# Kernel tuning notes

Hardware: AMD Instinct MI355X
Metric: run time of the kernel (lower is better)

## Reference

```python
import jax, jax.numpy as jnp
import numpy as np

B, L, D = 2, 2048, 1024
H = 16
DH = D // H
DFF = 4096
THETA = 10000.0
EPS = 1e-5


def setup_inputs() -> dict:
    key = jax.random.key(0)
    ks = jax.random.split(key, 6)
    s_qkv = (2.0 / (D + 3 * D)) ** 0.5
    s_o = (2.0 / (D + D)) ** 0.5
    s_ff = (2.0 / (D + DFF)) ** 0.5
    return {
        'x': jax.random.normal(ks[0], (B, L, D), jnp.float32),
        'w_qkv': jax.random.normal(ks[1], (3 * D, D), jnp.float32) * s_qkv,
        'w_o': jax.random.normal(ks[2], (D, D), jnp.float32) * s_o,
        'w1': jax.random.normal(ks[3], (DFF, D), jnp.float32) * s_ff,
        'w2': jax.random.normal(ks[4], (D, DFF), jnp.float32) * s_ff,
        'w3': jax.random.normal(ks[5], (DFF, D), jnp.float32) * s_ff,
        'g1': jnp.ones((D,), jnp.float32),
        'g2': jnp.ones((D,), jnp.float32),
    }


def _rmsnorm(x, g):
    xf = x.astype(jnp.float32)
    inv = jax.lax.rsqrt(jnp.mean(xf * xf, axis=-1, keepdims=True) + EPS)
    return (xf * inv * g).astype(x.dtype)


def _rotate_pair(t):
    # interleaved pairs: (x0,x1,x2,x3,...) -> (-x1,x0,-x3,x2,...)
    t2 = t.reshape(t.shape[:-1] + (t.shape[-1] // 2, 2))
    r = jnp.stack((-t2[..., 1], t2[..., 0]), axis=-1)
    return r.reshape(t.shape)


def reference(x, w_qkv, w_o, w1, w2, w3, g1, g2):
    Bb, Ll, Dd = x.shape
    # --- attention sublayer ---
    y = _rmsnorm(x, g1)
    qkv = y @ w_qkv.T                       # (B, L, 3D)
    q, k, v = jnp.split(qkv, 3, axis=-1)
    def to_heads(t):
        return t.reshape(Bb, Ll, H, DH).transpose(0, 2, 1, 3)  # (B,H,L,Dh)
    q, k, v = to_heads(q), to_heads(k), to_heads(v)
    # RoPE (interleaved), positions = 0..L-1
    inv_freq = 1.0 / (THETA ** (jnp.arange(0, DH, 2, dtype=jnp.float32) / DH))
    ang = jnp.arange(Ll, dtype=jnp.float32)[:, None] * inv_freq  # (L, Dh/2)
    ang = jnp.repeat(ang, 2, axis=-1)                            # (L, Dh)
    cos, sin = jnp.cos(ang), jnp.sin(ang)
    q = q * cos + _rotate_pair(q) * sin
    k = k * cos + _rotate_pair(k) * sin
    att = jnp.einsum('bhqd,bhkd->bhqk', q, k) * (1.0 / np.sqrt(DH))
    causal = jnp.tril(jnp.ones((Ll, Ll), dtype=bool))
    att = jnp.where(causal, att, -jnp.inf)
    att = jax.nn.softmax(att, axis=-1)
    yh = jnp.einsum('bhqk,bhkd->bhqd', att, v)
    y = yh.transpose(0, 2, 1, 3).reshape(Bb, Ll, Dd)
    x = x + y @ w_o.T
    # --- SwiGLU FFN sublayer ---
    y = _rmsnorm(x, g2)
    h = jax.nn.silu(y @ w1.T) * (y @ w3.T)
    return x + h @ w2.T
```

## Files before the change

kernel.cpp:

```cpp
#include <hip/hip_runtime.h>


typedef __attribute__((ext_vector_type(8))) short short8;
typedef __attribute__((ext_vector_type(4))) float f32x4;

#define DEV __device__ __forceinline__

DEV unsigned short f2b(float f) {
  unsigned int u = __builtin_bit_cast(unsigned int, f);
  unsigned int r = u + 0x7fffu + ((u >> 16) & 1u);
  return (unsigned short)(r >> 16);
}
DEV float b2f(unsigned short h) {
  return __builtin_bit_cast(float, ((unsigned int)h) << 16);
}
DEV f32x4 MFMA(short8 a, short8 b, f32x4 c) {
  return __builtin_amdgcn_mfma_f32_16x16x32_bf16(a, b, c, 0, 0, 0);
}
DEV void gload16(const void* g, void* lds) {
  __builtin_amdgcn_global_load_lds((const __attribute__((address_space(1))) void*)g,
                                   (__attribute__((address_space(3))) void*)lds, 16, 0, 0);
}

__global__ __launch_bounds__(256) void cvt_k(const float* __restrict__ src,
                                             unsigned short* __restrict__ dst, int n) {
  int i = (blockIdx.x * 256 + threadIdx.x) * 4;
  if (i + 3 < n) {
    float4 v = *(const float4*)(src + i);
    ushort4 o;
    o.x = f2b(v.x); o.y = f2b(v.y); o.z = f2b(v.z); o.w = f2b(v.w);
    *(ushort4*)(dst + i) = o;
  } else {
    for (int c = 0; c < 4 && i + c < n; ++c) dst[i + c] = f2b(src[i + c]);
  }
}

__global__ __launch_bounds__(256) void rope_k(float2* __restrict__ tab) {
  const int i = blockIdx.x * 256 + threadIdx.x;
  const int lt = i >> 5, pr = i & 31;
  const float invf = __expf((float)pr * -0.28782313662425572f);
  const float ang = (float)lt * invf;
  float sn, cs;
  sincosf(ang, &sn, &cs);
  tab[i] = make_float2(cs, sn);
}

__global__ __launch_bounds__(256) void rms_k(const float* __restrict__ x,
                                             const float* __restrict__ g,
                                             unsigned short* __restrict__ out) {
  const int row = blockIdx.x;
  const int t = threadIdx.x;
  const float4 v = *(const float4*)(x + (size_t)row * 1024 + t * 4);
  float ss = v.x * v.x + v.y * v.y + v.z * v.z + v.w * v.w;
#pragma unroll
  for (int m = 32; m >= 1; m >>= 1) ss += __shfl_xor(ss, m, 64);
  __shared__ float red[4];
  if ((t & 63) == 0) red[t >> 6] = ss;
  __syncthreads();
  float tot = red[0] + red[1] + red[2] + red[3];
  float inv = rsqrtf(tot * (1.0f / 1024.0f) + 1e-5f);
  ushort4 o;
  o.x = f2b(v.x * inv * g[t * 4 + 0]);
  o.y = f2b(v.y * inv * g[t * 4 + 1]);
  o.z = f2b(v.z * inv * g[t * 4 + 2]);
  o.w = f2b(v.w * inv * g[t * 4 + 3]);
  *(ushort4*)(out + (size_t)row * 1024 + t * 4) = o;
}

template <int MODE>
__global__ __launch_bounds__(256, 3) void gemm_bt(
    const unsigned short* __restrict__ A, const unsigned short* __restrict__ B0,
    int M, int N, int K,
    float* __restrict__ outF, const float* __restrict__ resid,
    unsigned short* __restrict__ q, unsigned short* __restrict__ k2,
    unsigned short* __restrict__ v,
    const float2* __restrict__ rtab) {
  __shared__ __align__(16) unsigned short As[2][128 * 32];
  __shared__ __align__(16) unsigned short Bs[2][128 * 32];
  const int t = threadIdx.x;
  const int wv = t >> 6, ln = t & 63;
  const int l15 = ln & 15, grp = ln >> 4;
  const int wr = wv >> 1, wc = wv & 1;
  int m0, n0;
  if constexpr (MODE == 1) {
    const int d = blockIdx.y * 8 + blockIdx.x;
    const int xcd = d & 7, j = d >> 3;
    m0 = (xcd * 4 + (j >> 3)) * 128;
    n0 = (j & 7) * 128;
  } else {
    m0 = blockIdx.y * 128;
    n0 = blockIdx.x * 128;
  }

  const char* sA0 = (const char*)A + ((size_t)(m0 + (t >> 2)) * K + (t & 3) * 8) * 2;
  const char* sA1 = (const char*)A + ((size_t)(m0 + 64 + (t >> 2)) * K + (t & 3) * 8) * 2;
  const char* sB0 = (const char*)B0 + ((size_t)(n0 + (t >> 2)) * K + (t & 3) * 8) * 2;
  const char* sB1 = (const char*)B0 + ((size_t)(n0 + 64 + (t >> 2)) * K + (t & 3) * 8) * 2;

  f32x4 acc[4][4];
#pragma unroll
  for (int mm = 0; mm < 4; ++mm)
#pragma unroll
    for (int nn = 0; nn < 4; ++nn) acc[mm][nn] = (f32x4){0.f, 0.f, 0.f, 0.f};

  const int KT = K >> 5;
  gload16(sA0, (char*)As[0] + wv * 1024);
  gload16(sA1, (char*)As[0] + 4096 + wv * 1024);
  gload16(sB0, (char*)Bs[0] + wv * 1024);
  gload16(sB1, (char*)Bs[0] + 4096 + wv * 1024);

#pragma unroll 1
  for (int kt = 0; kt < KT; ++kt) {
    const int par = kt & 1;
    const size_t ko = (size_t)((kt + 1 < KT) ? (kt + 1) : kt) * 64;
    gload16(sA0 + ko, (char*)As[par ^ 1] + wv * 1024);
    gload16(sA1 + ko, (char*)As[par ^ 1] + 4096 + wv * 1024);
    gload16(sB0 + ko, (char*)Bs[par ^ 1] + wv * 1024);
    gload16(sB1 + ko, (char*)Bs[par ^ 1] + 4096 + wv * 1024);
    asm volatile("s_waitcnt vmcnt(4)" ::: "memory");
    __builtin_amdgcn_s_barrier();
    const unsigned short* Ab = As[par];
    const unsigned short* Bb = Bs[par];
    short8 af[4], bf0[4];
#pragma unroll
    for (int mm = 0; mm < 4; ++mm)
      af[mm] = *(const short8*)&Ab[(wr * 64 + mm * 16 + l15) * 32 + grp * 8];
#pragma unroll
    for (int nn = 0; nn < 4; ++nn)
      bf0[nn] = *(const short8*)&Bb[(wc * 64 + nn * 16 + l15) * 32 + grp * 8];
#pragma unroll
    for (int mm = 0; mm < 4; ++mm)
#pragma unroll
      for (int nn = 0; nn < 4; ++nn) acc[mm][nn] = MFMA(af[mm], bf0[nn], acc[mm][nn]);
    __builtin_amdgcn_s_barrier();
  }

#pragma unroll
  for (int mm = 0; mm < 4; ++mm)
#pragma unroll
    for (int nn = 0; nn < 4; ++nn)
#pragma unroll
      for (int j = 0; j < 4; ++j) {
        const int r = m0 + wr * 64 + mm * 16 + grp * 4 + j;
        const int c = n0 + wc * 64 + nn * 16 + l15;
        float val = acc[mm][nn][j];
        if constexpr (MODE == 0) {
          const int mat = c >> 10;
          const int rem = c & 1023;
          const int hh = rem >> 6;
          const int dh = rem & 63;
          const int bt = r >> 11;
          const int lt = r & 2047;
          float outv = val;
          if (mat < 2) {
            const float partner = __shfl_xor(val, 1, 64);
            const float2 cs = rtab[lt * 32 + (dh >> 1)];
            outv = (dh & 1) ? (val * cs.x + partner * cs.y) : (val * cs.x - partner * cs.y);
          }
          unsigned short* dst = (mat == 0) ? q : ((mat == 1) ? k2 : v);
          dst[((size_t)(bt * 16 + hh) * 2048 + lt) * 64 + dh] = f2b(outv);
        } else {
          const size_t idx = (size_t)r * N + c;
          outF[idx] = resid[idx] + val;
        }
      }
}

__global__ __launch_bounds__(256, 3) void gemm_sk(
    const unsigned short* __restrict__ A, const unsigned short* __restrict__ B0,
    unsigned short* __restrict__ part) {
  __shared__ __align__(16) unsigned short As[2][128 * 32];
  __shared__ __align__(16) unsigned short Bs[2][128 * 32];
  const int t = threadIdx.x;
  const int wv = t >> 6, ln = t & 63;
  const int l15 = ln & 15, grp = ln >> 4;
  const int wr = wv >> 1, wc = wv & 1;
  const int d = blockIdx.y * 8 + blockIdx.x;
  const int xcd = d & 7, j = d >> 3;
  const int m0 = (xcd * 4 + (j >> 3)) * 128;
  const int n0 = (j & 7) * 128;
  const size_t kbase = (size_t)blockIdx.z * 1024;

  const char* sA0 = (const char*)A + ((size_t)(m0 + (t >> 2)) * 4096 + kbase + (t & 3) * 8) * 2;
  const char* sA1 = (const char*)A + ((size_t)(m0 + 64 + (t >> 2)) * 4096 + kbase + (t & 3) * 8) * 2;
  const char* sB0 = (const char*)B0 + ((size_t)(n0 + (t >> 2)) * 4096 + kbase + (t & 3) * 8) * 2;
  const char* sB1 = (const char*)B0 + ((size_t)(n0 + 64 + (t >> 2)) * 4096 + kbase + (t & 3) * 8) * 2;

  f32x4 acc[4][4];
#pragma unroll
  for (int mm = 0; mm < 4; ++mm)
#pragma unroll
    for (int nn = 0; nn < 4; ++nn) acc[mm][nn] = (f32x4){0.f, 0.f, 0.f, 0.f};

  gload16(sA0, (char*)As[0] + wv * 1024);
  gload16(sA1, (char*)As[0] + 4096 + wv * 1024);
  gload16(sB0, (char*)Bs[0] + wv * 1024);
  gload16(sB1, (char*)Bs[0] + 4096 + wv * 1024);

#pragma unroll 1
  for (int kt = 0; kt < 32; ++kt) {
    const int par = kt & 1;
    const size_t ko = (size_t)((kt + 1 < 32) ? (kt + 1) : kt) * 64;
    gload16(sA0 + ko, (char*)As[par ^ 1] + wv * 1024);
    gload16(sA1 + ko, (char*)As[par ^ 1] + 4096 + wv * 1024);
    gload16(sB0 + ko, (char*)Bs[par ^ 1] + wv * 1024);
    gload16(sB1 + ko, (char*)Bs[par ^ 1] + 4096 + wv * 1024);
    asm volatile("s_waitcnt vmcnt(4)" ::: "memory");
    __builtin_amdgcn_s_barrier();
    const unsigned short* Ab = As[par];
    const unsigned short* Bb = Bs[par];
    short8 af[4], bf0[4];
#pragma unroll
    for (int mm = 0; mm < 4; ++mm)
      af[mm] = *(const short8*)&Ab[(wr * 64 + mm * 16 + l15) * 32 + grp * 8];
#pragma unroll
    for (int nn = 0; nn < 4; ++nn)
      bf0[nn] = *(const short8*)&Bb[(wc * 64 + nn * 16 + l15) * 32 + grp * 8];
#pragma unroll
    for (int mm = 0; mm < 4; ++mm)
#pragma unroll
      for (int nn = 0; nn < 4; ++nn) acc[mm][nn] = MFMA(af[mm], bf0[nn], acc[mm][nn]);
    __builtin_amdgcn_s_barrier();
  }

  unsigned short* pz = part + (size_t)blockIdx.z * 4194304;
#pragma unroll
  for (int mm = 0; mm < 4; ++mm)
#pragma unroll
    for (int nn = 0; nn < 4; ++nn)
#pragma unroll
      for (int j = 0; j < 4; ++j) {
        const int r = m0 + wr * 64 + mm * 16 + grp * 4 + j;
        const int c = n0 + wc * 64 + nn * 16 + l15;
        pz[(size_t)r * 1024 + c] = f2b(acc[mm][nn][j]);
      }
}

__global__ __launch_bounds__(256) void red_k(const float* __restrict__ x2,
                                             const unsigned short* __restrict__ part,
                                             float* __restrict__ out) {
  const int i = (blockIdx.x * 256 + threadIdx.x) * 4;
  float4 r = *(const float4*)(x2 + i);
#pragma unroll
  for (int z = 0; z < 4; ++z) {
    const ushort4 p = *(const ushort4*)(part + (size_t)z * 4194304 + i);
    r.x += b2f(p.x);
    r.y += b2f(p.y);
    r.z += b2f(p.z);
    r.w += b2f(p.w);
  }
  *(float4*)(out + i) = r;
}

__global__ __launch_bounds__(512, 2) void ffn_k(
    const unsigned short* __restrict__ A, const unsigned short* __restrict__ B0,
    const unsigned short* __restrict__ B1, unsigned short* __restrict__ outH) {
  __shared__ __align__(16) char Asm[2][32768];
  __shared__ __align__(16) char Bsm[2][32768];
  const int t = threadIdx.x;
  const int wid = t >> 6, lane = t & 63;
  const int l15 = lane & 15, grp = lane >> 4;
  const int wr = wid >> 2, wc = wid & 3;
  const int m0 = blockIdx.y * 256;
  const int n0 = blockIdx.x * 256;

  const char* srcA[4];
  const char* srcB[4];
#pragma unroll
  for (int s = 0; s < 4; ++s) {
    const int lb = s * 8192 + t * 16;
    const int r = lb >> 7;
    const int sw = (((lb >> 4) & 7) * 16) ^ ((r & 7) << 4);
    srcA[s] = (const char*)A + (size_t)(m0 + r) * 2048 + sw;
    const int R = n0 + r;
    const unsigned short* bsrc = ((R >> 4) & 1) ? B1 : B0;
    const int br = ((R >> 5) << 4) + (R & 15);
    srcB[s] = (const char*)bsrc + (size_t)br * 2048 + sw;
  }

  f32x4 acc[8][4];
#pragma unroll
  for (int m = 0; m < 8; ++m)
#pragma unroll
    for (int n = 0; n < 4; ++n) acc[m][n] = (f32x4){0.f, 0.f, 0.f, 0.f};

  gload16(srcA[0], Asm[0] + 0 * 8192 + wid * 1024);
  gload16(srcA[1], Asm[0] + 1 * 8192 + wid * 1024);
  gload16(srcB[0], Bsm[0] + 0 * 8192 + wid * 1024);
  gload16(srcB[1], Bsm[0] + 1 * 8192 + wid * 1024);
  gload16(srcA[2], Asm[0] + 2 * 8192 + wid * 1024);
  gload16(srcA[3], Asm[0] + 3 * 8192 + wid * 1024);
  gload16(srcB[2], Bsm[0] + 2 * 8192 + wid * 1024);
  gload16(srcB[3], Bsm[0] + 3 * 8192 + wid * 1024);

  const int rA0 = wr * 64 + l15;
  const int rB0 = wc * 32 + l15;

#pragma unroll 1
  for (int kt = 0; kt < 16; ++kt) {
    const int cb = kt & 1;
    const size_t koff = (size_t)((kt + 1 < 16) ? (kt + 1) : kt) * 128;
    const char* Ab = Asm[cb];
    const char* Bb = Bsm[cb];
    char* An = Asm[cb ^ 1];
    char* Bn = Bsm[cb ^ 1];

    short8 a0[2][4], a1[2][4], b0[2][2], b1[2][2];

    gload16(srcA[0] + koff, An + 0 * 8192 + wid * 1024);
    gload16(srcA[1] + koff, An + 1 * 8192 + wid * 1024);
    asm volatile("s_waitcnt vmcnt(6)" ::: "memory");
    __builtin_amdgcn_s_barrier();
#pragma unroll
    for (int ks = 0; ks < 2; ++ks)
#pragma unroll
      for (int m = 0; m < 4; ++m) {
        const int r = rA0 + m * 16;
        a0[ks][m] = *(const short8*)(Ab + r * 128 + ((ks * 64 + grp * 16) ^ ((r & 7) << 4)));
      }
#pragma unroll
    for (int ks = 0; ks < 2; ++ks)
#pragma unroll
      for (int n = 0; n < 2; ++n) {
        const int r = rB0 + n * 16;
        b0[ks][n] = *(const short8*)(Bb + r * 128 + ((ks * 64 + grp * 16) ^ ((r & 7) << 4)));
      }
    __builtin_amdgcn_sched_barrier(0);
    __builtin_amdgcn_s_setprio(1);
#pragma unroll
    for (int ks = 0; ks < 2; ++ks)
#pragma unroll
      for (int m = 0; m < 4; ++m)
#pragma unroll
        for (int n = 0; n < 2; ++n) acc[m][n] = MFMA(a0[ks][m], b0[ks][n], acc[m][n]);
    __builtin_amdgcn_s_setprio(0);

    gload16(srcB[0] + koff, Bn + 0 * 8192 + wid * 1024);
    gload16(srcB[1] + koff, Bn + 1 * 8192 + wid * 1024);
    asm volatile("s_waitcnt vmcnt(4)" ::: "memory");
    __builtin_amdgcn_s_barrier();
#pragma unroll
    for (int ks = 0; ks < 2; ++ks)
#pragma unroll
      for (int n = 0; n < 2; ++n) {
        const int r = 128 + rB0 + n * 16;
        b1[ks][n] = *(const short8*)(Bb + r * 128 + ((ks * 64 + grp * 16) ^ ((r & 7) << 4)));
      }
    __builtin_amdgcn_sched_barrier(0);
    __builtin_amdgcn_s_setprio(1);
#pragma unroll
    for (int ks = 0; ks < 2; ++ks)
#pragma unroll
      for (int m = 0; m < 4; ++m)
#pragma unroll
        for (int n = 0; n < 2; ++n) acc[m][2 + n] = MFMA(a0[ks][m], b1[ks][n], acc[m][2 + n]);
    __builtin_amdgcn_s_setprio(0);

    gload16(srcA[2] + koff, An + 2 * 8192 + wid * 1024);
    gload16(srcA[3] + koff, An + 3 * 8192 + wid * 1024);
    __builtin_amdgcn_s_barrier();
#pragma unroll
    for (int ks = 0; ks < 2; ++ks)
#pragma unroll
      for (int m = 0; m < 4; ++m) {
        const int r = 128 + rA0 + m * 16;
        a1[ks][m] = *(const short8*)(Ab + r * 128 + ((ks * 64 + grp * 16) ^ ((r & 7) << 4)));
      }
    __builtin_amdgcn_sched_barrier(0);
    __builtin_amdgcn_s_setprio(1);
#pragma unroll
    for (int ks = 0; ks < 2; ++ks)
#pragma unroll
      for (int m = 0; m < 4; ++m)
#pragma unroll
        for (int n = 0; n < 2; ++n) acc[4 + m][2 + n] = MFMA(a1[ks][m], b1[ks][n], acc[4 + m][2 + n]);
    __builtin_amdgcn_s_setprio(0);

    gload16(srcB[2] + koff, Bn + 2 * 8192 + wid * 1024);
    gload16(srcB[3] + koff, Bn + 3 * 8192 + wid * 1024);
    __builtin_amdgcn_s_barrier();
    __builtin_amdgcn_s_setprio(1);
#pragma unroll
    for (int ks = 0; ks < 2; ++ks)
#pragma unroll
      for (int m = 0; m < 4; ++m)
#pragma unroll
        for (int n = 0; n < 2; ++n) acc[4 + m][n] = MFMA(a1[ks][m], b0[ks][n], acc[4 + m][n]);
    __builtin_amdgcn_s_setprio(0);
  }

#pragma unroll
  for (int mh = 0; mh < 2; ++mh)
#pragma unroll
    for (int m = 0; m < 4; ++m)
#pragma unroll
      for (int nh = 0; nh < 2; ++nh)
#pragma unroll
        for (int j = 0; j < 4; ++j) {
          const int row = m0 + mh * 128 + wr * 64 + m * 16 + grp * 4 + j;
          const int ch = (n0 >> 1) + nh * 64 + wc * 16 + l15;
          const float a1v = acc[mh * 4 + m][nh * 2 + 0][j];
          const float a3v = acc[mh * 4 + m][nh * 2 + 1][j];
          const float hval = a1v / (1.0f + __expf(-a1v)) * a3v;
          outH[(size_t)row * 4096 + ch] = f2b(hval);
        }
}

__global__ __launch_bounds__(256) void vtr_k(const unsigned short* __restrict__ v,
                                             unsigned short* __restrict__ vt) {
  __shared__ __align__(16) unsigned short tile[64][72];
  const int bh = blockIdx.y;
  const int lt0 = blockIdx.x * 64;
  const int t = threadIdx.x;
  const int r = t >> 2;
  const int c0 = (t & 3) * 16;
  const unsigned short* src = v + ((size_t)bh * 2048 + lt0 + r) * 64 + c0;
  *(short8*)&tile[r][c0] = *(const short8*)src;
  *(short8*)&tile[r][c0 + 8] = *(const short8*)(src + 8);
  __syncthreads();
  unsigned short outv[16];
#pragma unroll
  for (int i = 0; i < 16; ++i) outv[i] = tile[c0 + i][r];
  unsigned short* dst = vt + ((size_t)bh * 64 + r) * 2048 + lt0 + c0;
  *(short8*)dst = *(short8*)&outv[0];
  *(short8*)(dst + 8) = *(short8*)&outv[8];
}

__global__ __launch_bounds__(256) void attn_k(const unsigned short* __restrict__ qb,
                                              const unsigned short* __restrict__ kb,
                                              const unsigned short* __restrict__ vt,
                                              unsigned short* __restrict__ yh) {
  const int pair = blockIdx.x;
  const int bh = blockIdx.y;
  const int t = threadIdx.x;
  const int w = t >> 6, lane = t & 63;
  const int l15 = lane & 15, grp = lane >> 4;

  __shared__ __align__(16) char Ks[2][8192];
  __shared__ __align__(16) char Vs[2][8192];
  __shared__ __align__(16) char Ps[8192];
  char* Pw = Ps + w * 2048;

  const char* kg = (const char*)kb + (size_t)bh * 262144;
  const char* vg = (const char*)vt + (size_t)bh * 262144;

  const int lb0 = t * 16, lb1 = 4096 + t * 16;
  const int r0 = lb0 >> 7, r1 = lb1 >> 7;
  const int sl0 = (lb0 & 0x70) ^ ((r0 & 7) << 4);
  const int sl1 = (lb1 & 0x70) ^ ((r1 & 7) << 4);
  const char* srcK0 = kg + r0 * 128 + sl0;
  const char* srcK1 = kg + r1 * 128 + sl1;
  const char* srcV0 = vg + (size_t)r0 * 4096 + sl0;
  const char* srcV1 = vg + (size_t)r1 * 4096 + sl1;

  const int bq = bh >> 4, hh = bh & 15;

#pragma unroll 1
  for (int half = 0; half < 2; ++half) {
    const int qblk = half ? pair : (31 - pair);
    const int qw = qblk * 64 + w * 16;

    const unsigned short* qp = qb + ((size_t)bh * 2048 + qw) * 64;
    const short8 qf0 = *(const short8*)(qp + l15 * 64 + grp * 8);
    const short8 qf1 = *(const short8*)(qp + l15 * 64 + 32 + grp * 8);

    f32x4 o[4];
#pragma unroll
    for (int d = 0; d < 4; ++d) o[d] = (f32x4){0.f, 0.f, 0.f, 0.f};
    float mrun[4], lrun[4];
#pragma unroll
    for (int j = 0; j < 4; ++j) { mrun[j] = -3.0e38f; lrun[j] = 0.f; }

    const int nkt = qblk + 1;

    __syncthreads();
    {
      gload16(srcK0, Ks[0] + w * 1024);
      gload16(srcK1, Ks[0] + 4096 + w * 1024);
      gload16(srcV0, Vs[0] + w * 1024);
      gload16(srcV1, Vs[0] + 4096 + w * 1024);
    }

#pragma unroll 1
    for (int kt = 0; kt < nkt; ++kt) {
      const int par = kt & 1;
      const int ktn = (kt + 1 < nkt) ? (kt + 1) : kt;
      gload16(srcK0 + (size_t)ktn * 8192, Ks[par ^ 1] + w * 1024);
      gload16(srcK1 + (size_t)ktn * 8192, Ks[par ^ 1] + 4096 + w * 1024);
      gload16(srcV0 + ktn * 128, Vs[par ^ 1] + w * 1024);
      gload16(srcV1 + ktn * 128, Vs[par ^ 1] + 4096 + w * 1024);
      asm volatile("s_waitcnt vmcnt(4)" ::: "memory");
      __builtin_amdgcn_s_barrier();

      const char* Kc = Ks[par];
      const char* Vc = Vs[par];

      f32x4 s[4];
#pragma unroll
      for (int c = 0; c < 4; ++c) {
        const int r = c * 16 + l15;
        const int xr = (r & 7) << 4;
        const short8 kf0 = *(const short8*)(Kc + r * 128 + ((grp * 16) ^ xr));
        const short8 kf1 = *(const short8*)(Kc + r * 128 + ((64 + grp * 16) ^ xr));
        f32x4 z = (f32x4){0.f, 0.f, 0.f, 0.f};
        __builtin_amdgcn_s_setprio(1);
        z = MFMA(qf0, kf0, z);
        z = MFMA(qf1, kf1, z);
        __builtin_amdgcn_s_setprio(0);
        s[c] = z;
      }

      const bool diag = (kt == qblk);
      float alpha[4], p[4][4];
#pragma unroll
      for (int j = 0; j < 4; ++j) {
        const int qg = qw + grp * 4 + j;
        float a[4];
#pragma unroll
        for (int c = 0; c < 4; ++c) {
          float av = s[c][j] * 0.125f;
          if (diag && (kt * 64 + c * 16 + l15 > qg)) av = -3.0e38f;
          a[c] = av;
        }
        float mx = fmaxf(fmaxf(a[0], a[1]), fmaxf(a[2], a[3]));
        mx = fmaxf(mx, __shfl_xor(mx, 1, 64));
        mx = fmaxf(mx, __shfl_xor(mx, 2, 64));
        mx = fmaxf(mx, __shfl_xor(mx, 4, 64));
        mx = fmaxf(mx, __shfl_xor(mx, 8, 64));
        const float mnew = fmaxf(mrun[j], mx);
        alpha[j] = __expf(mrun[j] - mnew);
        mrun[j] = mnew;
        float rs = 0.f;
#pragma unroll
        for (int c = 0; c < 4; ++c) {
          const float e = __expf(a[c] - mnew);
          p[c][j] = e;
          rs += e;
        }
        rs += __shfl_xor(rs, 1, 64);
        rs += __shfl_xor(rs, 2, 64);
        rs += __shfl_xor(rs, 4, 64);
        rs += __shfl_xor(rs, 8, 64);
        lrun[j] = lrun[j] * alpha[j] + rs;
      }
#pragma unroll
      for (int d = 0; d < 4; ++d)
#pragma unroll
        for (int j = 0; j < 4; ++j) o[d][j] *= alpha[j];

#pragma unroll
      for (int j = 0; j < 4; ++j) {
        const int r = grp * 4 + j;
        const int xr = (r & 7) << 4;
        char* pr = Pw + r * 128;
#pragma unroll
        for (int c = 0; c < 4; ++c)
          *(unsigned short*)(pr + (((c * 16 + l15) * 2) ^ xr)) = f2b(p[c][j]);
      }
      const int xp = (l15 & 7) << 4;
      const short8 pa0 = *(const short8*)(Pw + l15 * 128 + ((grp * 16) ^ xp));
      const short8 pa1 = *(const short8*)(Pw + l15 * 128 + ((64 + grp * 16) ^ xp));
#pragma unroll
      for (int db = 0; db < 4; ++db) {
        const int rv = db * 16 + l15;
        const int xv = (rv & 7) << 4;
        const short8 vf0 = *(const short8*)(Vc + rv * 128 + ((grp * 16) ^ xv));
        const short8 vf1 = *(const short8*)(Vc + rv * 128 + ((64 + grp * 16) ^ xv));
        __builtin_amdgcn_s_setprio(1);
        o[db] = MFMA(pa0, vf0, o[db]);
        o[db] = MFMA(pa1, vf1, o[db]);
        __builtin_amdgcn_s_setprio(0);
      }
      __builtin_amdgcn_s_barrier();
    }

#pragma unroll
    for (int db = 0; db < 4; ++db)
#pragma unroll
      for (int j = 0; j < 4; ++j) {
        const float valo = o[db][j] / lrun[j];
        const size_t rowo = (size_t)bq * 2048 + qw + grp * 4 + j;
        yh[rowo * 1024 + hh * 64 + db * 16 + l15] = f2b(valo);
      }
  }
}

extern "C" void kernel_launch(void* const* d_in, const int* in_sizes, int n_in,
                              void* d_out, int out_size, void* d_ws, size_t ws_size,
                              hipStream_t stream) {
  const float* x = (const float*)d_in[0];
  const float* wqkv = (const float*)d_in[1];
  const float* wo = (const float*)d_in[2];
  const float* w1 = (const float*)d_in[3];
  const float* w2 = (const float*)d_in[4];
  const float* w3 = (const float*)d_in[5];
  const float* g1 = (const float*)d_in[6];
  const float* g2 = (const float*)d_in[7];

  char* ws = (char*)d_ws;
  unsigned short* wqkv_b = (unsigned short*)(ws + 0);
  unsigned short* wo_b = (unsigned short*)(ws + 6291456);
  unsigned short* w1_b = (unsigned short*)(ws + 8388608);
  unsigned short* w3_b = (unsigned short*)(ws + 16777216);
  unsigned short* yb = (unsigned short*)(ws + 25165824);
  float* x2 = (float*)(ws + 33554432);
  float2* rtab = (float2*)(ws + 33554432);
  unsigned short* w2_b = (unsigned short*)(ws + 50331648);
  unsigned short* qb = (unsigned short*)(ws + 58720256);
  unsigned short* kb = (unsigned short*)(ws + 67108864);
  unsigned short* vb = (unsigned short*)(ws + 75497472);
  unsigned short* vt = (unsigned short*)(ws + 83886080);
  unsigned short* yh = vb;
  unsigned short* hb = (unsigned short*)(ws + 58720256);
  unsigned short* part = (unsigned short*)(ws + 0);
  if (ws_size < 92274688) return;

  cvt_k<<<3072, 256, 0, stream>>>(wqkv, wqkv_b, 3145728);
  cvt_k<<<1024, 256, 0, stream>>>(wo, wo_b, 1048576);
  cvt_k<<<4096, 256, 0, stream>>>(w1, w1_b, 4194304);
  cvt_k<<<4096, 256, 0, stream>>>(w3, w3_b, 4194304);
  cvt_k<<<4096, 256, 0, stream>>>(w2, w2_b, 4194304);
  rope_k<<<256, 256, 0, stream>>>(rtab);

  rms_k<<<4096, 256, 0, stream>>>(x, g1, yb);
  gemm_bt<0><<<dim3(24, 32), 256, 0, stream>>>(yb, wqkv_b, 4096, 3072, 1024,
                                               nullptr, nullptr, qb, kb, vb, rtab);
  vtr_k<<<dim3(32, 32), 256, 0, stream>>>(vb, vt);
  attn_k<<<dim3(16, 32), 256, 0, stream>>>(qb, kb, vt, yh);
  gemm_bt<1><<<dim3(8, 32), 256, 0, stream>>>(yh, wo_b, 4096, 1024, 1024,
                                              x2, x, nullptr, nullptr, nullptr, nullptr);
  rms_k<<<4096, 256, 0, stream>>>(x2, g2, yb);
  ffn_k<<<dim3(32, 16), 512, 0, stream>>>(yb, w1_b, w3_b, hb);
  gemm_sk<<<dim3(8, 32, 4), 256, 0, stream>>>(hb, w2_b, part);
  red_k<<<4096, 256, 0, stream>>>(x2, part, (float*)d_out);
}
```

Baseline: 303.4 us.

## Restructure attention softmax with transposed scores, exp2 prescaling and lazy rescale

The 1/sqrt(d)*log2(e) factor is folded into Q in the QKV epilogue, so softmax can use exp2 directly. Scores are computed as K·Q^T, which gives each lane one query row and lets the row max and sum reduce with two cross-lane shuffles instead of four per row. The output rescale is skipped when no row max changes, and P is packed to bf16 with v_cvt_pk_bf16_f32 and written with vector stores. Attention blocks are also remapped to a 1D grid that groups heads per XCD for better L2 locality. Folding the scale into Q before bf16 rounding slightly changes numerics.

```diff
diff --git a/kernel.cpp b/kernel.cpp
--- a/kernel.cpp
+++ b/kernel.cpp
@@ -13,6 +13,11 @@
 }
 DEV float b2f(unsigned short h) {
   return __builtin_bit_cast(float, ((unsigned int)h) << 16);
+}
+DEV unsigned int cvtpk(float lo, float hi) {
+  unsigned int r;
+  asm("v_cvt_pk_bf16_f32 %0, %1, %2" : "=v"(r) : "v"(lo), "v"(hi));
+  return r;
 }
 DEV f32x4 MFMA(short8 a, short8 b, f32x4 c) {
   return __builtin_amdgcn_mfma_f32_16x16x32_bf16(a, b, c, 0, 0, 0);
@@ -157,6 +162,7 @@
             const float2 cs = rtab[lt * 32 + (dh >> 1)];
             outv = (dh & 1) ? (val * cs.x + partner * cs.y) : (val * cs.x - partner * cs.y);
           }
+          if (mat == 0) outv *= 0.18033688011112042f;
           unsigned short* dst = (mat == 0) ? q : ((mat == 1) ? k2 : v);
           dst[((size_t)(bt * 16 + hh) * 2048 + lt) * 64 + dh] = f2b(outv);
         } else {
@@ -430,8 +436,10 @@
                                               const unsigned short* __restrict__ kb,
                                               const unsigned short* __restrict__ vt,
                                               unsigned short* __restrict__ yh) {
-  const int pair = blockIdx.x;
-  const int bh = blockIdx.y;
+  const int dd = blockIdx.x;
+  const int xcd = dd & 7, idx = dd >> 3;
+  const int bh = xcd + 8 * (idx & 3);
+  const int pair = idx >> 2;
   const int t = threadIdx.x;
   const int w = t >> 6, lane = t & 63;
   const int l15 = lane & 15, grp = lane >> 4;
@@ -467,9 +475,7 @@
     f32x4 o[4];
 #pragma unroll
     for (int d = 0; d < 4; ++d) o[d] = (f32x4){0.f, 0.f, 0.f, 0.f};
-    float mrun[4], lrun[4];
-#pragma unroll
-    for (int j = 0; j < 4; ++j) { mrun[j] = -3.0e38f; lrun[j] = 0.f; }
+    float mrun = -3.0e38f, lrun = 0.f;
 
     const int nkt = qblk + 1;
 
@@ -495,7 +501,7 @@
       const char* Kc = Ks[par];
       const char* Vc = Vs[par];
 
-      f32x4 s[4];
+      f32x4 st[4];
 #pragma unroll
       for (int c = 0; c < 4; ++c) {
         const int r = c * 16 + l15;
@@ -504,62 +510,69 @@
         const short8 kf1 = *(const short8*)(Kc + r * 128 + ((64 + grp * 16) ^ xr));
         f32x4 z = (f32x4){0.f, 0.f, 0.f, 0.f};
         __builtin_amdgcn_s_setprio(1);
-        z = MFMA(qf0, kf0, z);
-        z = MFMA(qf1, kf1, z);
+        z = MFMA(kf0, qf0, z);
+        z = MFMA(kf1, qf1, z);
         __builtin_amdgcn_s_setprio(0);
-        s[c] = z;
+        st[c] = z;
       }
 
       const bool diag = (kt == qblk);
-      float alpha[4], p[4][4];
-#pragma unroll
-      for (int j = 0; j < 4; ++j) {
-        const int qg = qw + grp * 4 + j;
-        float a[4];
-#pragma unroll
-        for (int c = 0; c < 4; ++c) {
-          float av = s[c][j] * 0.125f;
-          if (diag && (kt * 64 + c * 16 + l15 > qg)) av = -3.0e38f;
-          a[c] = av;
+      const int qg = qw + l15;
+      float av[4][4];
+      float tm = -3.0e38f;
+#pragma unroll
+      for (int c = 0; c < 4; ++c)
+#pragma unroll
+        for (int j = 0; j < 4; ++j) {
+          float x = st[c][j];
+          if (diag) {
+            const int kg2 = kt * 64 + c * 16 + grp * 4 + j;
+            if (kg2 > qg) x = -3.0e38f;
+          }
+          av[c][j] = x;
+          tm = fmaxf(tm, x);
         }
-        float mx = fmaxf(fmaxf(a[0], a[1]), fmaxf(a[2], a[3]));
-        mx = fmaxf(mx, __shfl_xor(mx, 1, 64));
-        mx = fmaxf(mx, __shfl_xor(mx, 2, 64));
-        mx = fmaxf(mx, __shfl_xor(mx, 4, 64));
-        mx = fmaxf(mx, __shfl_xor(mx, 8, 64));
-        const float mnew = fmaxf(mrun[j], mx);
-        alpha[j] = __expf(mrun[j] - mnew);
-        mrun[j] = mnew;
-        float rs = 0.f;
-#pragma unroll
-        for (int c = 0; c < 4; ++c) {
-          const float e = __expf(a[c] - mnew);
-          p[c][j] = e;
-          rs += e;
-        }
-        rs += __shfl_xor(rs, 1, 64);
-        rs += __shfl_xor(rs, 2, 64);
-        rs += __shfl_xor(rs, 4, 64);
-        rs += __shfl_xor(rs, 8, 64);
-        lrun[j] = lrun[j] * alpha[j] + rs;
-      }
-#pragma unroll
-      for (int d = 0; d < 4; ++d)
-#pragma unroll
-        for (int j = 0; j < 4; ++j) o[d][j] *= alpha[j];
-
-#pragma unroll
-      for (int j = 0; j < 4; ++j) {
-        const int r = grp * 4 + j;
-        const int xr = (r & 7) << 4;
-        char* pr = Pw + r * 128;
-#pragma unroll
-        for (int c = 0; c < 4; ++c)
-          *(unsigned short*)(pr + (((c * 16 + l15) * 2) ^ xr)) = f2b(p[c][j]);
-      }
+      tm = fmaxf(tm, __shfl_xor(tm, 16, 64));
+      tm = fmaxf(tm, __shfl_xor(tm, 32, 64));
+
+      const float mold = mrun;
+      const bool need = tm > mold;
+      mrun = fmaxf(mold, tm);
+      const float aown = need ? __builtin_amdgcn_exp2f(mold - mrun) : 1.0f;
+      if (__any(need)) {
+        float am[4];
+#pragma unroll
+        for (int j = 0; j < 4; ++j) am[j] = __shfl(aown, grp * 4 + j, 64);
+#pragma unroll
+        for (int d = 0; d < 4; ++d)
+#pragma unroll
+          for (int j = 0; j < 4; ++j) o[d][j] *= am[j];
+      }
+
+      float rs = 0.f;
+      uint2 pk[4];
+#pragma unroll
+      for (int c = 0; c < 4; ++c) {
+        const float p0 = __builtin_amdgcn_exp2f(av[c][0] - mrun);
+        const float p1 = __builtin_amdgcn_exp2f(av[c][1] - mrun);
+        const float p2 = __builtin_amdgcn_exp2f(av[c][2] - mrun);
+        const float p3 = __builtin_amdgcn_exp2f(av[c][3] - mrun);
+        rs += (p0 + p1) + (p2 + p3);
+        pk[c].x = cvtpk(p0, p1);
+        pk[c].y = cvtpk(p2, p3);
+      }
+      rs += __shfl_xor(rs, 16, 64);
+      rs += __shfl_xor(rs, 32, 64);
+      lrun = lrun * aown + rs;
+
       const int xp = (l15 & 7) << 4;
-      const short8 pa0 = *(const short8*)(Pw + l15 * 128 + ((grp * 16) ^ xp));
-      const short8 pa1 = *(const short8*)(Pw + l15 * 128 + ((64 + grp * 16) ^ xp));
+      char* prow = Pw + l15 * 128;
+#pragma unroll
+      for (int c = 0; c < 4; ++c)
+        *(uint2*)(prow + ((32 * c + 8 * grp) ^ xp)) = pk[c];
+
+      const short8 pa0 = *(const short8*)(prow + ((grp * 16) ^ xp));
+      const short8 pa1 = *(const short8*)(prow + ((64 + grp * 16) ^ xp));
 #pragma unroll
       for (int db = 0; db < 4; ++db) {
         const int rv = db * 16 + l15;
@@ -574,11 +587,14 @@
       __builtin_amdgcn_s_barrier();
     }
 
+    float lr[4];
+#pragma unroll
+    for (int j = 0; j < 4; ++j) lr[j] = __shfl(lrun, grp * 4 + j, 64);
 #pragma unroll
     for (int db = 0; db < 4; ++db)
 #pragma unroll
       for (int j = 0; j < 4; ++j) {
-        const float valo = o[db][j] / lrun[j];
+        const float valo = o[db][j] / lr[j];
         const size_t rowo = (size_t)bq * 2048 + qw + grp * 4 + j;
         yh[rowo * 1024 + hh * 64 + db * 16 + l15] = f2b(valo);
       }
@@ -626,7 +642,7 @@
   gemm_bt<0><<<dim3(24, 32), 256, 0, stream>>>(yb, wqkv_b, 4096, 3072, 1024,
                                                nullptr, nullptr, qb, kb, vb, rtab);
   vtr_k<<<dim3(32, 32), 256, 0, stream>>>(vb, vt);
-  attn_k<<<dim3(16, 32), 256, 0, stream>>>(qb, kb, vt, yh);
+  attn_k<<<dim3(512), 256, 0, stream>>>(qb, kb, vt, yh);
   gemm_bt<1><<<dim3(8, 32), 256, 0, stream>>>(yh, wo_b, 4096, 1024, 1024,
                                               x2, x, nullptr, nullptr, nullptr, nullptr);
   rms_k<<<4096, 256, 0, stream>>>(x2, g2, yb);
```

New measurement: 282.6 us. 6.9% less time.
